# Optimization experiments

Hardware: AMD Instinct MI355X
Metric: run time of the kernel (lower is better)

The kernel has to match this reference:

```python
import jax, jax.numpy as jnp
import numpy as np

N_NODES = 100000
N_EDGES = 200000
N_FEAT = 300
HIDDEN = 300
NUM_GRAPHS = 2048
NUM_BOND_TYPE = 6
NUM_BOND_DIR = 3


def setup_inputs() -> dict:
    key = jax.random.key(0)
    ks = jax.random.split(key, 12)
    x = jax.random.normal(ks[0], (N_NODES, N_FEAT), dtype=jnp.float32)
    edge_index = jax.random.randint(ks[1], (2, N_EDGES), 0, N_NODES, dtype=jnp.int64)
    edge_attr = jax.random.randint(ks[2], (N_EDGES, 2), 0, NUM_BOND_DIR, dtype=jnp.int64)
    batch = jnp.sort(jax.random.randint(ks[3], (N_NODES,), 0, NUM_GRAPHS, dtype=jnp.int64))
    s = 1.0 / np.sqrt(N_FEAT)
    emb1 = jax.random.normal(ks[4], (NUM_BOND_TYPE, N_FEAT), dtype=jnp.float32) * s
    emb2 = jax.random.normal(ks[5], (NUM_BOND_DIR, N_FEAT), dtype=jnp.float32) * s
    W1 = jax.random.normal(ks[6], (N_FEAT, 2 * N_FEAT), dtype=jnp.float32) * s
    b1 = jnp.zeros((2 * N_FEAT,), dtype=jnp.float32)
    W2 = jax.random.normal(ks[7], (2 * N_FEAT, HIDDEN), dtype=jnp.float32) * (1.0 / np.sqrt(2 * N_FEAT))
    b2 = jnp.zeros((HIDDEN,), dtype=jnp.float32)
    Wfc = jax.random.normal(ks[8], (HIDDEN, HIDDEN), dtype=jnp.float32) * (1.0 / np.sqrt(HIDDEN))
    bfc = jnp.zeros((HIDDEN,), dtype=jnp.float32)
    return {"x": x, "edge_index": edge_index, "edge_attr": edge_attr, "batch": batch,
            "emb1": emb1, "emb2": emb2, "W1": W1, "b1": b1, "W2": W2, "b2": b2,
            "Wfc": Wfc, "bfc": bfc}


def reference(x, edge_index, edge_attr, batch, emb1, emb2, W1, b1, W2, b2, Wfc, bfc):
    n = x.shape[0]
    # add_self_loops(fill_value=0): append N self edges with zero edge_attr
    loop = jnp.arange(n, dtype=edge_index.dtype)
    src = jnp.concatenate([edge_index[0], loop])  # [E+N]
    dst = jnp.concatenate([edge_index[1], loop])
    ea = jnp.concatenate([edge_attr, jnp.zeros((n, 2), dtype=edge_attr.dtype)], axis=0)
    # edge embeddings (shared by both conv layers)
    edge_emb = emb1[ea[:, 0]] + emb2[ea[:, 1]]  # [E+N, F]

    def mlp(h):
        return jax.nn.relu(h @ W1 + b1) @ W2 + b2

    def gin(h):
        # message: x_j + edge_emb, scatter-add at target nodes, then shared MLP
        msg = h[src] + edge_emb
        aggr = jax.ops.segment_sum(msg, dst, num_segments=n)
        return mlp(aggr)

    h = jax.nn.relu(gin(x))
    h = jax.nn.relu(gin(h))
    # global_add_pool over graphs in batch
    g = jax.ops.segment_sum(h, batch, num_segments=NUM_GRAPHS)  # [G, H]
    return g @ Wfc + bfc
```

## Files before the change

kernel.cpp:

```cpp
#include <hip/hip_runtime.h>
#include <hip/hip_bf16.h>

#define NFEAT 300
#define KP 320
#define NGRAPH 2048
#define N1P 640
#define N2P 384
#define NTD 18
#define SCAN_B 2048

typedef __bf16 bf16x8 __attribute__((ext_vector_type(8)));
typedef float  f32x4  __attribute__((ext_vector_type(4)));
typedef unsigned short u16x8 __attribute__((ext_vector_type(8)));

__device__ __forceinline__ unsigned short f2b(float v) {
    union { float f; unsigned u; } x; x.f = v;
    unsigned r = x.u + 0x7fff + ((x.u >> 16) & 1);
    return (unsigned short)(r >> 16);
}
__device__ __forceinline__ float b2f(unsigned short u) {
    union { unsigned u; float f; } x; x.u = ((unsigned)u) << 16;
    return x.f;
}

#define GLD_LDS16(g, l)                                                        \
    __builtin_amdgcn_global_load_lds(                                          \
        (const __attribute__((address_space(1))) void*)(g),                    \
        (__attribute__((address_space(3))) void*)(l), 16, 0, 0)

__device__ __forceinline__ void cvtW_body(
    const float* __restrict__ W, unsigned short* __restrict__ Wt,
    int rows, int cols, int Kpad, int Npad, int t)
{
    if (t >= Npad * Kpad) return;
    int nn = t / Kpad, k = t % Kpad;
    float v = (k < rows && nn < cols) ? W[(size_t)k * cols + nn] : 0.f;
    Wt[t] = f2b(v);
}

__global__ __launch_bounds__(256) void k_prep(
    const float* __restrict__ W1, unsigned short* __restrict__ Wt1,
    const float* __restrict__ W2, unsigned short* __restrict__ Wt2,
    const float* __restrict__ emb1, const float* __restrict__ emb2,
    float* __restrict__ embc,
    const float* __restrict__ x, unsigned short* __restrict__ xb,
    int* __restrict__ deg, int n, int Mpad,
    int b1e, int b2e, int b3e, int b4e)
{
    int b = blockIdx.x, tid = threadIdx.x;
    if (b < b1e) {
        cvtW_body(W1, Wt1, NFEAT, 600, KP, N1P, b * 256 + tid);
    } else if (b < b2e) {
        cvtW_body(W2, Wt2, 600, NFEAT, N1P, N2P, (b - b1e) * 256 + tid);
    } else if (b < b3e) {
        int t = (b - b2e) * 256 + tid;
        if (t < NTD * KP) {
            int td = t / KP, c = t % KP;
            int t1 = td / 3, d = td % 3;
            embc[t] = (c < NFEAT) ? emb1[t1 * NFEAT + c] + emb2[d * NFEAT + c] : 0.f;
        }
    } else if (b < b4e) {
        int idx = (b - b3e) * 256 + tid;
        if (idx < Mpad * (KP / 8)) {
            int row = idx / (KP / 8), c0 = (idx % (KP / 8)) * 8;
            unsigned short o[8];
#pragma unroll
            for (int j = 0; j < 8; ++j) {
                int col = c0 + j;
                float v = (row < n && col < NFEAT) ? x[(size_t)row * NFEAT + col] : 0.f;
                o[j] = f2b(v);
            }
            *(uint4*)&xb[(size_t)row * KP + c0] = *(uint4*)o;
        }
    } else {
        int i = (b - b4e) * 256 + tid;
        if (i < n) deg[i] = 0;
    }
}

__global__ __launch_bounds__(256) void k_deg(
    const int* __restrict__ ei, int* __restrict__ deg, int E)
{
    int e = blockIdx.x * blockDim.x + threadIdx.x;
    if (e >= E) return;
    atomicAdd(&deg[ei[E + e]], 1);
}

__global__ __launch_bounds__(256) void k_scan1(
    const int* __restrict__ deg, int* __restrict__ offsets,
    int* __restrict__ bsum, int n)
{
    __shared__ int sh[256];
    int tid = threadIdx.x;
    int base = blockIdx.x * SCAN_B + tid * 8;
    int v[8], run = 0;
#pragma unroll
    for (int j = 0; j < 8; ++j) {
        int i = base + j;
        v[j] = (i < n) ? deg[i] : 0;
        run += v[j];
        v[j] = run;
    }
    sh[tid] = run;
    __syncthreads();
    for (int off = 1; off < 256; off <<= 1) {
        int t = (tid >= off) ? sh[tid - off] : 0;
        __syncthreads();
        sh[tid] += t;
        __syncthreads();
    }
    int excl = sh[tid] - run;
#pragma unroll
    for (int j = 0; j < 8; ++j) {
        int i = base + j;
        if (i < n) offsets[i + 1] = excl + v[j];
    }
    if (tid == 0) bsum[blockIdx.x] = sh[255];
}

__global__ __launch_bounds__(256) void k_scan3(
    const int* __restrict__ deg, int* __restrict__ offsets,
    const int* __restrict__ bsum, int* __restrict__ cursor, int n)
{
    int i = blockIdx.x * blockDim.x + threadIdx.x;
    if (i == 0) offsets[0] = 0;
    if (i >= n) return;
    int nbi = i / SCAN_B;
    int pre = 0;
    for (int j = 0; j < nbi; ++j) pre += bsum[j];
    int fin = offsets[i + 1] + pre;
    offsets[i + 1] = fin;
    cursor[i] = fin - deg[i];
}

__global__ __launch_bounds__(256) void k_fill(
    const int* __restrict__ ei, const int* __restrict__ ea,
    int* __restrict__ cursor, int* __restrict__ edgerec, int E)
{
    int e = blockIdx.x * blockDim.x + threadIdx.x;
    if (e >= E) return;
    int dst = ei[E + e];
    int pos = atomicAdd(&cursor[dst], 1);
    int src = ei[e];
    int td  = ea[2 * e] * 3 + ea[2 * e + 1];
    edgerec[pos] = src | (td << 20);
}

__global__ __launch_bounds__(256) void k_aggr(
    const unsigned short* __restrict__ h,
    const int* __restrict__ offsets, const int* __restrict__ edgerec,
    const float* __restrict__ embc,
    unsigned short* __restrict__ Ab, int n, int Mpad)
{
    int idx = blockIdx.x * blockDim.x + threadIdx.x;
    if (idx >= Mpad * (KP / 16)) return;
    int v = idx / (KP / 16), c0 = (idx % (KP / 16)) * 16;
    unsigned short* outp = &Ab[(size_t)v * KP + c0];
    if (v >= n) {
        *(uint4*)outp       = make_uint4(0, 0, 0, 0);
        *(uint4*)(outp + 8) = make_uint4(0, 0, 0, 0);
        return;
    }
    float acc[16];
    const unsigned short* hr = &h[(size_t)v * KP + c0];
    u16x8 hv0 = *(const u16x8*)hr;
    u16x8 hv1 = *(const u16x8*)(hr + 8);
    const float* e0 = embc + c0;
#pragma unroll
    for (int j = 0; j < 8; ++j) {
        acc[j]     = b2f(hv0[j]) + e0[j];
        acc[8 + j] = b2f(hv1[j]) + e0[8 + j];
    }

    int beg = offsets[v], end = offsets[v + 1];
    for (int e = beg; e < end; ++e) {
        int rec = edgerec[e];
        int src = rec & 0xFFFFF;
        int td  = rec >> 20;
        const unsigned short* hs = &h[(size_t)src * KP + c0];
        u16x8 s0 = *(const u16x8*)hs;
        u16x8 s1 = *(const u16x8*)(hs + 8);
        const float* ee = embc + td * KP + c0;
#pragma unroll
        for (int j = 0; j < 8; ++j) {
            acc[j]     += b2f(s0[j]) + ee[j];
            acc[8 + j] += b2f(s1[j]) + ee[8 + j];
        }
    }
    unsigned short o[16];
#pragma unroll
    for (int j = 0; j < 16; ++j) o[j] = f2b(acc[j]);
    *(uint4*)outp       = *(uint4*)o;
    *(uint4*)(outp + 8) = *(uint4*)(o + 8);
}

__global__ __launch_bounds__(256) void k_gemm(
    const unsigned short* __restrict__ Ag, const unsigned short* __restrict__ Bg,
    const float* __restrict__ bias, int bias_n,
    unsigned short* __restrict__ C, int ldc, int store_cols,
    int K, int npass, int MT)
{
    __shared__ unsigned short smem[24576];

    int tid  = threadIdx.x;
    int lane = tid & 63, wave = tid >> 6;

    int l    = blockIdx.x;
    int xcd  = l & 7;
    int j    = l >> 3;
    int ncol = j % npass;
    int panel= (j / npass) * 8 + xcd;
    if (panel >= MT) return;
    int m0 = panel * 128;

    int wm = (wave >> 1) * 64, wn = (wave & 1) * 64;
    int fr = lane & 15, fq = lane >> 4;
    int colq = lane & 15, rq = (lane >> 4) * 4;

    const unsigned short* Abase = Ag + (size_t)m0 * K;
    const unsigned short* Bbase = Bg + (size_t)ncol * 128 * K;

    int c0 = tid, c1 = 256 + tid;
    size_t aoff0 = (size_t)(c0 >> 2) * K + 8 * ((c0 & 3) ^ ((c0 >> 3) & 3));
    size_t aoff1 = (size_t)(c1 >> 2) * K + 8 * ((c1 & 3) ^ ((c1 >> 3) & 3));

    int fswz = 8 * (fq ^ ((fr >> 1) & 3));

#define STAGEK(bi, kt_) do {                                                   \
        int _b  = (bi) * 8192;                                                 \
        int _k0 = (kt_) * 32;                                                  \
        GLD_LDS16(Abase + aoff0 + _k0, &smem[_b + c0 * 8]);                    \
        GLD_LDS16(Abase + aoff1 + _k0, &smem[_b + c1 * 8]);                    \
        GLD_LDS16(Bbase + aoff0 + _k0, &smem[_b + 4096 + c0 * 8]);             \
        GLD_LDS16(Bbase + aoff1 + _k0, &smem[_b + 4096 + c1 * 8]);             \
    } while (0)

#define SBAR() do {                                                            \
        __builtin_amdgcn_sched_barrier(0);                                     \
        __builtin_amdgcn_s_barrier();                                          \
        __builtin_amdgcn_sched_barrier(0);                                     \
    } while (0)

    f32x4 acc[4][4];
#pragma unroll
    for (int i = 0; i < 4; ++i)
#pragma unroll
        for (int jj = 0; jj < 4; ++jj)
            acc[i][jj] = (f32x4){0.f, 0.f, 0.f, 0.f};

    int NT = K >> 5;
    STAGEK(0, 0);
    STAGEK(1, 1);

    for (int kt = 0; kt < NT; ++kt) {
        int base = (kt % 3) * 8192;

        if (kt + 1 < NT) {
            asm volatile("s_waitcnt vmcnt(4)" ::: "memory");
        } else {
            asm volatile("s_waitcnt vmcnt(0)" ::: "memory");
        }
        SBAR();

        if (kt + 2 < NT) STAGEK((kt + 2) % 3, kt + 2);

        bf16x8 af[4], bfv[4];
#pragma unroll
        for (int i = 0; i < 4; ++i) {
            af[i]  = *(const bf16x8*)&smem[base + (wm + i * 16 + fr) * 32 + fswz];
            bfv[i] = *(const bf16x8*)&smem[base + 4096 + (wn + i * 16 + fr) * 32 + fswz];
        }
#pragma unroll
        for (int i = 0; i < 4; ++i)
#pragma unroll
            for (int jj = 0; jj < 4; ++jj)
                acc[i][jj] = __builtin_amdgcn_mfma_f32_16x16x32_bf16(
                    af[i], bfv[jj], acc[i][jj], 0, 0, 0);
    }
    __syncthreads();

#pragma unroll
    for (int ch = 0; ch < 2; ++ch) {
        if ((wn >> 6) == ch) {
#pragma unroll
            for (int jj = 0; jj < 4; ++jj) {
                int lc  = jj * 16 + colq;
                int col = ncol * 128 + wn + jj * 16 + colq;
                float bv = (col < bias_n) ? bias[col] : 0.f;
#pragma unroll
                for (int i = 0; i < 4; ++i) {
                    int rbase = wm + i * 16 + rq;
#pragma unroll
                    for (int r = 0; r < 4; ++r) {
                        float v = fmaxf(acc[i][jj][r] + bv, 0.f);
                        smem[(rbase + r) * 64 + lc] = f2b(v);
                    }
                }
            }
        }
        __syncthreads();
        int cbase = ncol * 128 + ch * 64;
        if (cbase < store_cols) {
#pragma unroll
            for (int i = 0; i < 4; ++i) {
                int idx = i * 256 + tid;
                int row = idx >> 3, c8 = idx & 7;
                *(uint4*)&C[(size_t)(m0 + row) * ldc + cbase + c8 * 8] =
                    *(uint4*)&smem[row * 64 + c8 * 8];
            }
        }
        __syncthreads();
    }
#undef STAGEK
#undef SBAR
}

__global__ __launch_bounds__(256) void k_pool(
    const unsigned short* __restrict__ H, const int* __restrict__ batch,
    float* __restrict__ g, int n)
{
    __shared__ float red[3][KP];
    int gid  = blockIdx.x;
    int tid  = threadIdx.x;
    int wave = tid >> 6, lane = tid & 63;
    int c0   = lane * 8;

    int lo = 0, hi = n;
    while (lo < hi) { int mid = (lo + hi) >> 1; if (batch[mid] < gid) lo = mid + 1; else hi = mid; }
    int start = lo;
    hi = n;
    while (lo < hi) { int mid = (lo + hi) >> 1; if (batch[mid] < gid + 1) lo = mid + 1; else hi = mid; }
    int end = lo;

    float acc[8] = {0.f, 0.f, 0.f, 0.f, 0.f, 0.f, 0.f, 0.f};
    if (c0 < KP) {
        for (int v = start + wave; v < end; v += 4) {
            u16x8 hv = *(const u16x8*)&H[(size_t)v * KP + c0];
#pragma unroll
            for (int j = 0; j < 8; ++j) acc[j] += b2f(hv[j]);
        }
        if (wave != 0) {
#pragma unroll
            for (int j = 0; j < 8; ++j) red[wave - 1][c0 + j] = acc[j];
        }
    }
    __syncthreads();
    if (wave == 0 && c0 < NFEAT) {
#pragma unroll
        for (int j = 0; j < 8; ++j) {
            if (c0 + j < NFEAT) {
                float s = acc[j] + red[0][c0 + j] + red[1][c0 + j] + red[2][c0 + j];
                g[(size_t)gid * NFEAT + c0 + j] = s;
            }
        }
    }
}

__global__ __launch_bounds__(256) void k_final(
    const float* __restrict__ g, const float* __restrict__ Wfc,
    const float* __restrict__ bfc, float* __restrict__ out)
{
    int idx = blockIdx.x * blockDim.x + threadIdx.x;
    if (idx >= NGRAPH * NFEAT) return;
    int r = idx / NFEAT, c = idx % NFEAT;
    const float* gr = &g[(size_t)r * NFEAT];
    float s0 = 0.f, s1 = 0.f, s2 = 0.f, s3 = 0.f;
    for (int k = 0; k < NFEAT; k += 4) {
        s0 = fmaf(gr[k],     Wfc[(size_t)(k)     * NFEAT + c], s0);
        s1 = fmaf(gr[k + 1], Wfc[(size_t)(k + 1) * NFEAT + c], s1);
        s2 = fmaf(gr[k + 2], Wfc[(size_t)(k + 2) * NFEAT + c], s2);
        s3 = fmaf(gr[k + 3], Wfc[(size_t)(k + 3) * NFEAT + c], s3);
    }
    out[idx] = bfc[c] + ((s0 + s1) + (s2 + s3));
}

extern "C" void kernel_launch(void* const* d_in, const int* in_sizes, int n_in,
                              void* d_out, int out_size, void* d_ws, size_t ws_size,
                              hipStream_t stream)
{
    const float* x    = (const float*)d_in[0];
    const int*   ei   = (const int*)  d_in[1];
    const int*   ea   = (const int*)  d_in[2];
    const int*   batch= (const int*)  d_in[3];
    const float* emb1 = (const float*)d_in[4];
    const float* emb2 = (const float*)d_in[5];
    const float* W1   = (const float*)d_in[6];
    const float* b1   = (const float*)d_in[7];
    const float* W2   = (const float*)d_in[8];
    const float* b2   = (const float*)d_in[9];
    const float* Wfc  = (const float*)d_in[10];
    const float* bfc  = (const float*)d_in[11];
    float* out = (float*)d_out;

    int n = in_sizes[0] / NFEAT;
    int E = in_sizes[1] / 2;
    int MT   = (n + 127) / 128;
    int Mpad = MT * 128;
    int MT8  = ((MT + 7) / 8) * 8;

    char* p = (char*)d_ws;
    auto take = [&](size_t bytes) { char* r = p; p += (bytes + 255) & ~(size_t)255; return r; };
    unsigned short* T    = (unsigned short*)take((size_t)Mpad * N1P * 2);
    unsigned short* xb   = T;
    unsigned short* Ab   = (unsigned short*)take((size_t)Mpad * KP * 2);
    unsigned short* Hb   = (unsigned short*)take((size_t)Mpad * KP * 2);
    unsigned short* Wt1  = (unsigned short*)take((size_t)N1P * KP * 2);
    unsigned short* Wt2  = (unsigned short*)take((size_t)N2P * N1P * 2);
    float*          embc = (float*)take((size_t)NTD * KP * 4);
    float*          g    = (float*)take((size_t)NGRAPH * NFEAT * 4);
    int*            deg  = (int*)take((size_t)n * 4);
    int*            offs = (int*)take((size_t)(n + 1) * 4);
    int*            curs = (int*)take((size_t)n * 4);
    int*            erec = (int*)take((size_t)E * 4);
    int*            bsum = (int*)take(256 * 4);

    dim3 blk(256);
    int nb = (n + SCAN_B - 1) / SCAN_B;

    int nb1 = (N1P * KP + 255) / 256;
    int nb2 = (N2P * N1P + 255) / 256;
    int nb3 = (NTD * KP + 255) / 256;
    int nb4 = (Mpad * (KP / 8) + 255) / 256;
    int nb5 = (n + 255) / 256;
    int b1e = nb1, b2e = b1e + nb2, b3e = b2e + nb3, b4e = b3e + nb4;
    k_prep<<<b4e + nb5, blk, 0, stream>>>(W1, Wt1, W2, Wt2, emb1, emb2, embc,
                                          x, xb, deg, n, Mpad, b1e, b2e, b3e, b4e);

    k_deg  <<<(E + 255) / 256, blk, 0, stream>>>(ei, deg, E);
    k_scan1<<<nb, blk, 0, stream>>>(deg, offs, bsum, n);
    k_scan3<<<(n + 255) / 256, blk, 0, stream>>>(deg, offs, bsum, curs, n);
    k_fill <<<(E + 255) / 256, blk, 0, stream>>>(ei, ea, curs, erec, E);

    int aggrBlocks = (Mpad * (KP / 16) + 255) / 256;

    k_aggr<<<aggrBlocks, blk, 0, stream>>>(xb, offs, erec, embc, Ab, n, Mpad);
    k_gemm<<<MT8 * (N1P / 128), blk, 0, stream>>>(Ab, Wt1, b1, 600, T, N1P, N1P, KP, N1P / 128, MT);
    k_gemm<<<MT8 * (N2P / 128), blk, 0, stream>>>(T, Wt2, b2, NFEAT, Hb, KP, KP, N1P, N2P / 128, MT);

    k_aggr<<<aggrBlocks, blk, 0, stream>>>(Hb, offs, erec, embc, Ab, n, Mpad);
    k_gemm<<<MT8 * (N1P / 128), blk, 0, stream>>>(Ab, Wt1, b1, 600, T, N1P, N1P, KP, N1P / 128, MT);
    k_gemm<<<MT8 * (N2P / 128), blk, 0, stream>>>(T, Wt2, b2, NFEAT, Hb, KP, KP, N1P, N2P / 128, MT);

    k_pool <<<NGRAPH, blk, 0, stream>>>(Hb, batch, g, n);
    k_final<<<(NGRAPH * NFEAT + 255) / 256, blk, 0, stream>>>(g, Wfc, bfc, out);
}
```

Before: 662.3 us.

## Enlarge GEMM block tile to 256 rows for better B reuse

Doubles the GEMM block tile in M from 128 to 256 rows. Each wave now computes a 128x64 sub-tile with 8x4 MFMA accumulators, and the LDS staging buffers grow to match. More MFMA work is done per B fragment loaded, cutting LDS and global traffic per flop and halving the block count. In exchange the accumulator register use doubles, which can lower occupancy, and LDS per block rises to 72KB.

```diff
diff --git a/kernel.cpp b/kernel.cpp
--- a/kernel.cpp
+++ b/kernel.cpp
@@ -200,7 +200,7 @@
     unsigned short* __restrict__ C, int ldc, int store_cols,
     int K, int npass, int MT)
 {
-    __shared__ unsigned short smem[24576];
+    __shared__ unsigned short smem[36864];
 
     int tid  = threadIdx.x;
     int lane = tid & 63, wave = tid >> 6;
@@ -211,28 +211,29 @@
     int ncol = j % npass;
     int panel= (j / npass) * 8 + xcd;
     if (panel >= MT) return;
-    int m0 = panel * 128;
-
-    int wm = (wave >> 1) * 64, wn = (wave & 1) * 64;
+    int m0 = panel * 256;
+
+    int wm = (wave >> 1) * 128, wn = (wave & 1) * 64;
     int fr = lane & 15, fq = lane >> 4;
     int colq = lane & 15, rq = (lane >> 4) * 4;
 
     const unsigned short* Abase = Ag + (size_t)m0 * K;
     const unsigned short* Bbase = Bg + (size_t)ncol * 128 * K;
 
-    int c0 = tid, c1 = 256 + tid;
-    size_t aoff0 = (size_t)(c0 >> 2) * K + 8 * ((c0 & 3) ^ ((c0 >> 3) & 3));
-    size_t aoff1 = (size_t)(c1 >> 2) * K + 8 * ((c1 & 3) ^ ((c1 >> 3) & 3));
+    size_t aoffA = (size_t)(tid >> 2) * K + 8 * ((tid & 3) ^ ((tid >> 3) & 3));
+    size_t rowK64 = (size_t)64 * K;
 
     int fswz = 8 * (fq ^ ((fr >> 1) & 3));
 
 #define STAGEK(bi, kt_) do {                                                   \
-        int _b  = (bi) * 8192;                                                 \
+        int _b  = (bi) * 12288;                                                \
         int _k0 = (kt_) * 32;                                                  \
-        GLD_LDS16(Abase + aoff0 + _k0, &smem[_b + c0 * 8]);                    \
-        GLD_LDS16(Abase + aoff1 + _k0, &smem[_b + c1 * 8]);                    \
-        GLD_LDS16(Bbase + aoff0 + _k0, &smem[_b + 4096 + c0 * 8]);             \
-        GLD_LDS16(Bbase + aoff1 + _k0, &smem[_b + 4096 + c1 * 8]);             \
+        GLD_LDS16(Abase + aoffA + _k0,              &smem[_b + tid * 8]);      \
+        GLD_LDS16(Abase + aoffA + rowK64 + _k0,     &smem[_b + (tid + 256) * 8]); \
+        GLD_LDS16(Abase + aoffA + 2 * rowK64 + _k0, &smem[_b + (tid + 512) * 8]); \
+        GLD_LDS16(Abase + aoffA + 3 * rowK64 + _k0, &smem[_b + (tid + 768) * 8]); \
+        GLD_LDS16(Bbase + aoffA + _k0,              &smem[_b + 8192 + tid * 8]); \
+        GLD_LDS16(Bbase + aoffA + rowK64 + _k0,     &smem[_b + 8192 + (tid + 256) * 8]); \
     } while (0)
 
 #define SBAR() do {                                                            \
@@ -241,9 +242,9 @@
         __builtin_amdgcn_sched_barrier(0);                                     \
     } while (0)
 
-    f32x4 acc[4][4];
-#pragma unroll
-    for (int i = 0; i < 4; ++i)
+    f32x4 acc[8][4];
+#pragma unroll
+    for (int i = 0; i < 8; ++i)
 #pragma unroll
         for (int jj = 0; jj < 4; ++jj)
             acc[i][jj] = (f32x4){0.f, 0.f, 0.f, 0.f};
@@ -253,10 +254,10 @@
     STAGEK(1, 1);
 
     for (int kt = 0; kt < NT; ++kt) {
-        int base = (kt % 3) * 8192;
+        int base = (kt % 3) * 12288;
 
         if (kt + 1 < NT) {
-            asm volatile("s_waitcnt vmcnt(4)" ::: "memory");
+            asm volatile("s_waitcnt vmcnt(6)" ::: "memory");
         } else {
             asm volatile("s_waitcnt vmcnt(0)" ::: "memory");
         }
@@ -264,14 +265,15 @@
 
         if (kt + 2 < NT) STAGEK((kt + 2) % 3, kt + 2);
 
-        bf16x8 af[4], bfv[4];
-#pragma unroll
-        for (int i = 0; i < 4; ++i) {
+        bf16x8 af[8], bfv[4];
+#pragma unroll
+        for (int i = 0; i < 8; ++i)
             af[i]  = *(const bf16x8*)&smem[base + (wm + i * 16 + fr) * 32 + fswz];
-            bfv[i] = *(const bf16x8*)&smem[base + 4096 + (wn + i * 16 + fr) * 32 + fswz];
-        }
-#pragma unroll
-        for (int i = 0; i < 4; ++i)
+#pragma unroll
+        for (int jj = 0; jj < 4; ++jj)
+            bfv[jj] = *(const bf16x8*)&smem[base + 8192 + (wn + jj * 16 + fr) * 32 + fswz];
+#pragma unroll
+        for (int i = 0; i < 8; ++i)
 #pragma unroll
             for (int jj = 0; jj < 4; ++jj)
                 acc[i][jj] = __builtin_amdgcn_mfma_f32_16x16x32_bf16(
@@ -279,17 +281,18 @@
     }
     __syncthreads();
 
+    int wc = wave & 1, wr = wave >> 1;
 #pragma unroll
     for (int ch = 0; ch < 2; ++ch) {
-        if ((wn >> 6) == ch) {
+        if (wc == ch) {
 #pragma unroll
             for (int jj = 0; jj < 4; ++jj) {
                 int lc  = jj * 16 + colq;
-                int col = ncol * 128 + wn + jj * 16 + colq;
+                int col = ncol * 128 + ch * 64 + jj * 16 + colq;
                 float bv = (col < bias_n) ? bias[col] : 0.f;
 #pragma unroll
-                for (int i = 0; i < 4; ++i) {
-                    int rbase = wm + i * 16 + rq;
+                for (int i = 0; i < 8; ++i) {
+                    int rbase = wr * 128 + i * 16 + rq;
 #pragma unroll
                     for (int r = 0; r < 4; ++r) {
                         float v = fmaxf(acc[i][jj][r] + bv, 0.f);
@@ -302,8 +305,8 @@
         int cbase = ncol * 128 + ch * 64;
         if (cbase < store_cols) {
 #pragma unroll
-            for (int i = 0; i < 4; ++i) {
-                int idx = i * 256 + tid;
+            for (int q = 0; q < 8; ++q) {
+                int idx = q * 256 + tid;
                 int row = idx >> 3, c8 = idx & 7;
                 *(uint4*)&C[(size_t)(m0 + row) * ldc + cbase + c8 * 8] =
                     *(uint4*)&smem[row * 64 + c8 * 8];
@@ -394,8 +397,8 @@
 
     int n = in_sizes[0] / NFEAT;
     int E = in_sizes[1] / 2;
-    int MT   = (n + 127) / 128;
-    int Mpad = MT * 128;
+    int MT   = (n + 255) / 256;
+    int Mpad = MT * 256;
     int MT8  = ((MT + 7) / 8) * 8;
 
     char* p = (char*)d_ws;
```

New measurement: 785.2 us. +18.5%, slower.

## Deepen GEMM prefetch to four stages and fuse pooling with final FC

Applied to the files above, without the earlier changes.

The GEMM kernel's LDS ring buffer grows from three to four stages. It now prefetches three K-tiles ahead, with vmcnt waits adjusted to match, so more global-load latency is hidden. The pool and final FC kernels are merged: each graph block reduces its rows into shared memory and then computes the 300-wide output row directly, removing one launch and the g intermediate round trip. The cost is a larger LDS footprint in the GEMM, which may reduce occupancy, and a serial 300-step FC loop per block.

```diff
diff --git a/kernel.cpp b/kernel.cpp
--- a/kernel.cpp
+++ b/kernel.cpp
@@ -200,7 +200,7 @@
     unsigned short* __restrict__ C, int ldc, int store_cols,
     int K, int npass, int MT)
 {
-    __shared__ unsigned short smem[24576];
+    __shared__ unsigned short smem[32768];
 
     int tid  = threadIdx.x;
     int lane = tid & 63, wave = tid >> 6;
@@ -251,18 +251,21 @@
     int NT = K >> 5;
     STAGEK(0, 0);
     STAGEK(1, 1);
+    STAGEK(2, 2);
 
     for (int kt = 0; kt < NT; ++kt) {
-        int base = (kt % 3) * 8192;
-
-        if (kt + 1 < NT) {
+        int base = (kt & 3) * 8192;
+
+        if (kt < NT - 2) {
+            asm volatile("s_waitcnt vmcnt(8)" ::: "memory");
+        } else if (kt < NT - 1) {
             asm volatile("s_waitcnt vmcnt(4)" ::: "memory");
         } else {
             asm volatile("s_waitcnt vmcnt(0)" ::: "memory");
         }
         SBAR();
 
-        if (kt + 2 < NT) STAGEK((kt + 2) % 3, kt + 2);
+        if (kt + 3 < NT) STAGEK((kt + 3) & 3, kt + 3);
 
         bf16x8 af[4], bfv[4];
 #pragma unroll
@@ -315,11 +318,13 @@
 #undef SBAR
 }
 
-__global__ __launch_bounds__(256) void k_pool(
+__global__ __launch_bounds__(256) void k_poolfc(
     const unsigned short* __restrict__ H, const int* __restrict__ batch,
-    float* __restrict__ g, int n)
+    const float* __restrict__ Wfc, const float* __restrict__ bfc,
+    float* __restrict__ out, int n)
 {
     __shared__ float red[3][KP];
+    __shared__ float grow[KP];
     int gid  = blockIdx.x;
     int tid  = threadIdx.x;
     int wave = tid >> 6, lane = tid & 63;
@@ -345,33 +350,23 @@
         }
     }
     __syncthreads();
-    if (wave == 0 && c0 < NFEAT) {
-#pragma unroll
-        for (int j = 0; j < 8; ++j) {
-            if (c0 + j < NFEAT) {
-                float s = acc[j] + red[0][c0 + j] + red[1][c0 + j] + red[2][c0 + j];
-                g[(size_t)gid * NFEAT + c0 + j] = s;
-            }
-        }
-    }
-}
-
-__global__ __launch_bounds__(256) void k_final(
-    const float* __restrict__ g, const float* __restrict__ Wfc,
-    const float* __restrict__ bfc, float* __restrict__ out)
-{
-    int idx = blockIdx.x * blockDim.x + threadIdx.x;
-    if (idx >= NGRAPH * NFEAT) return;
-    int r = idx / NFEAT, c = idx % NFEAT;
-    const float* gr = &g[(size_t)r * NFEAT];
-    float s0 = 0.f, s1 = 0.f, s2 = 0.f, s3 = 0.f;
-    for (int k = 0; k < NFEAT; k += 4) {
-        s0 = fmaf(gr[k],     Wfc[(size_t)(k)     * NFEAT + c], s0);
-        s1 = fmaf(gr[k + 1], Wfc[(size_t)(k + 1) * NFEAT + c], s1);
-        s2 = fmaf(gr[k + 2], Wfc[(size_t)(k + 2) * NFEAT + c], s2);
-        s3 = fmaf(gr[k + 3], Wfc[(size_t)(k + 3) * NFEAT + c], s3);
-    }
-    out[idx] = bfc[c] + ((s0 + s1) + (s2 + s3));
+    if (wave == 0 && c0 < KP) {
+#pragma unroll
+        for (int j = 0; j < 8; ++j)
+            grow[c0 + j] = acc[j] + red[0][c0 + j] + red[1][c0 + j] + red[2][c0 + j];
+    }
+    __syncthreads();
+
+    float s0 = 0.f, s1 = 0.f;
+    int cA = tid, cB = tid + 256;
+    for (int k = 0; k < NFEAT; ++k) {
+        float gk = grow[k];
+        const float* wr = &Wfc[(size_t)k * NFEAT];
+        if (cA < NFEAT) s0 = fmaf(gk, wr[cA], s0);
+        if (cB < NFEAT) s1 = fmaf(gk, wr[cB], s1);
+    }
+    if (cA < NFEAT) out[(size_t)gid * NFEAT + cA] = s0 + bfc[cA];
+    if (cB < NFEAT) out[(size_t)gid * NFEAT + cB] = s1 + bfc[cB];
 }
 
 extern "C" void kernel_launch(void* const* d_in, const int* in_sizes, int n_in,
@@ -407,7 +402,6 @@
     unsigned short* Wt1  = (unsigned short*)take((size_t)N1P * KP * 2);
     unsigned short* Wt2  = (unsigned short*)take((size_t)N2P * N1P * 2);
     float*          embc = (float*)take((size_t)NTD * KP * 4);
-    float*          g    = (float*)take((size_t)NGRAPH * NFEAT * 4);
     int*            deg  = (int*)take((size_t)n * 4);
     int*            offs = (int*)take((size_t)(n + 1) * 4);
     int*            curs = (int*)take((size_t)n * 4);
@@ -441,6 +435,5 @@
     k_gemm<<<MT8 * (N1P / 128), blk, 0, stream>>>(Ab, Wt1, b1, 600, T, N1P, N1P, KP, N1P / 128, MT);
     k_gemm<<<MT8 * (N2P / 128), blk, 0, stream>>>(T, Wt2, b2, NFEAT, Hb, KP, KP, N1P, N2P / 128, MT);
 
-    k_pool <<<NGRAPH, blk, 0, stream>>>(Hb, batch, g, n);
-    k_final<<<(NGRAPH * NFEAT + 255) / 256, blk, 0, stream>>>(g, Wfc, bfc, out);
-}
+    k_poolfc<<<NGRAPH, blk, 0, stream>>>(Hb, batch, Wfc, bfc, out, n);
+}
```

New measurement: 855.1 us. +29.1%, slower.
